# Performance work log

Hardware: AMD Instinct MI355X
Metric: run time of the kernel (lower is better)

The kernel has to match this reference:

```python
import jax, jax.numpy as jnp
import numpy as np
from jax import lax

N, C, A, H, W = 32, 512, 256, 64, 64

def _maxpool2(t):
    # 2x2 max pool, stride 2, NCHW
    return lax.reduce_window(t, -jnp.inf, lax.max, (1, 1, 2, 2), (1, 1, 2, 2), 'VALID')

def setup_inputs() -> dict:
    key = jax.random.key(0)
    ks = jax.random.split(key, 5)
    return {
        'x': jax.random.normal(ks[0], (N, C, H, W), dtype=jnp.float32),
        'w_g': jax.random.normal(ks[1], (A, C), dtype=jnp.float32) * 0.02,
        'b_g': jax.random.normal(ks[2], (A,), dtype=jnp.float32) * 0.02,
        'w_phi': jax.random.normal(ks[3], (A, C), dtype=jnp.float32) * 0.02,
        'b_phi': jax.random.normal(ks[4], (A,), dtype=jnp.float32) * 0.02,
    }

def reference(x, w_g, b_g, w_phi, b_phi):
    n, c, h, w = x.shape
    # g: 1x1 conv in->attn, flattened spatial: (N, A, H*W)
    g_x = (jnp.einsum('nchw,ac->nahw', x, w_g) + b_g[None, :, None, None]).reshape(n, A, h * w)
    # theta: maxpool of x, (N, C, HW/4)
    theta_x = _maxpool2(x).reshape(n, c, -1)
    # phi: 1x1 conv then maxpool, (N, HW/4, A)
    phi_conv = jnp.einsum('nchw,ac->nahw', x, w_phi) + b_phi[None, :, None, None]
    phi_x = _maxpool2(phi_conv).reshape(n, A, -1)  # (N, A, HW/4)
    # channel-attention scores: (N, C, A)
    cmat = jnp.einsum('ncm,nam->nca', theta_x, phi_x)
    attn = jax.nn.softmax(cmat, axis=-1)
    # aggregate: (N, C, HW)
    y = jnp.einsum('nca,nal->ncl', attn, g_x)
    z = y.reshape(n, c, h, w)
    return z + x
```

## Files before the change

### kernel.cpp

```cpp
#include <hip/hip_runtime.h>


typedef _Float16 half8 __attribute__((ext_vector_type(8)));
typedef _Float16 half4v __attribute__((ext_vector_type(4)));
typedef float f32x4 __attribute__((ext_vector_type(4)));

#define NB 32
#define CD 512
#define AD 256
#define PD 4096
#define PPD 1024

#define OFF_XT    0UL
#define OFF_WC    134217728UL
#define OFF_THETA 134742016UL
#define OFF_GT    168296448UL
#define OFF_PHI   235405312UL
#define OFF_ATTN  252182528UL

__global__ __launch_bounds__(256) void k_prep_w(const float* __restrict__ w_g,
                                                const float* __restrict__ w_phi,
                                                _Float16* __restrict__ Wc) {
    int idx4 = blockIdx.x * 256 + threadIdx.x;
    int flat = idx4 * 4;
    const float* src = (flat < AD * CD) ? (w_g + flat) : (w_phi + (flat - AD * CD));
    float4 v = *(const float4*)src;
    half4v h;
    h[0] = (_Float16)v.x; h[1] = (_Float16)v.y; h[2] = (_Float16)v.z; h[3] = (_Float16)v.w;
    *(half4v*)(Wc + flat) = h;
}

__global__ __launch_bounds__(256) void k_prep_x(const float* __restrict__ x,
                                                _Float16* __restrict__ xT,
                                                _Float16* __restrict__ theta) {
    __shared__ _Float16 tile[32 * 136];
    int pb = blockIdx.x;
    int cb = blockIdx.y;
    int n  = blockIdx.z;
    int t  = threadIdx.x;
    int p0 = pb * 128, c0 = cb * 32;

    const float* xbase = x + ((size_t)n * CD + c0) * PD + p0;
#pragma unroll
    for (int i = 0; i < 4; ++i) {
        int idx = i * 256 + t;
        int cl = idx >> 5;
        int ch = idx & 31;
        float4 v = *(const float4*)(xbase + (size_t)cl * PD + ch * 4);
        half4v h;
        h[0] = (_Float16)v.x; h[1] = (_Float16)v.y; h[2] = (_Float16)v.z; h[3] = (_Float16)v.w;
        *(half4v*)&tile[cl * 136 + ch * 4] = h;
    }
    __syncthreads();

    {
        int pl = t >> 1, ch = t & 1;
        _Float16 vals[16] __attribute__((aligned(16)));
#pragma unroll
        for (int j = 0; j < 16; ++j) vals[j] = tile[(ch * 16 + j) * 136 + pl];
        _Float16* dst = xT + ((size_t)n * PD + p0 + pl) * CD + c0 + ch * 16;
        *(uint4*)dst       = *(uint4*)&vals[0];
        *(uint4*)(dst + 8) = *(uint4*)&vals[8];
    }
    {
        int cl = t >> 3, u0 = (t & 7) * 4;
        _Float16 o[4] __attribute__((aligned(8)));
#pragma unroll
        for (int j = 0; j < 4; ++j) {
            int w2 = (u0 + j) * 2;
            float a0 = (float)tile[cl * 136 + w2];
            float a1 = (float)tile[cl * 136 + w2 + 1];
            float a2 = (float)tile[cl * 136 + 64 + w2];
            float a3 = (float)tile[cl * 136 + 64 + w2 + 1];
            o[j] = (_Float16)fmaxf(fmaxf(a0, a1), fmaxf(a2, a3));
        }
        _Float16* dst = theta + ((size_t)n * CD + c0 + cl) * PPD + pb * 32 + u0;
        *(uint2*)dst = *(uint2*)&o[0];
    }
}

__global__ __launch_bounds__(256) void k_gemm1(const _Float16* __restrict__ Wc,
                                               const _Float16* __restrict__ xT,
                                               const float* __restrict__ b_g,
                                               const float* __restrict__ b_phi,
                                               _Float16* __restrict__ gT,
                                               _Float16* __restrict__ phi) {
    __shared__ _Float16 smem[17408];
    _Float16* As = smem;
    _Float16* Bs = smem + 5120;

    int pb = blockIdx.x, ab = blockIdx.y, n = blockIdx.z;
    int a0 = ab * 128, p0 = pb * 128;
    int t = threadIdx.x;
    int w = t >> 6, l = t & 63;
    int ln = l & 15, q = l >> 4;
    int mw = (w >> 1) * 64, nw = (w & 1) * 64;

    const f32x4 vzero = {0.f, 0.f, 0.f, 0.f};
    f32x4 acc[4][4];
#pragma unroll
    for (int i = 0; i < 4; ++i)
#pragma unroll
        for (int j = 0; j < 4; ++j) acc[i][j] = vzero;

    const _Float16* Abase = Wc + (size_t)a0 * CD;
    const _Float16* Bbase = xT + ((size_t)n * PD + p0) * CD;

    for (int k0 = 0; k0 < 512; k0 += 32) {
#pragma unroll
        for (int i = 0; i < 2; ++i) {
            int idx = i * 256 + t;
            int row = idx >> 2, ch = idx & 3;
            *(half8*)&As[row * 40 + ch * 8] = *(const half8*)(Abase + (size_t)row * CD + k0 + ch * 8);
            *(half8*)&Bs[row * 40 + ch * 8] = *(const half8*)(Bbase + (size_t)row * CD + k0 + ch * 8);
        }
        __syncthreads();
        half8 af[4], bf[4];
#pragma unroll
        for (int mt = 0; mt < 4; ++mt) af[mt] = *(const half8*)&As[(mw + mt * 16 + ln) * 40 + q * 8];
#pragma unroll
        for (int nt = 0; nt < 4; ++nt) bf[nt] = *(const half8*)&Bs[(nw + nt * 16 + ln) * 40 + q * 8];
#pragma unroll
        for (int mt = 0; mt < 4; ++mt)
#pragma unroll
            for (int nt = 0; nt < 4; ++nt)
                acc[mt][nt] = __builtin_amdgcn_mfma_f32_16x16x32_f16(af[mt], bf[nt], acc[mt][nt], 0, 0, 0);
        __syncthreads();
    }

    bool is_g = (a0 < 256);
    const float* bias = is_g ? b_g : b_phi;
    int abase = a0 - (is_g ? 0 : 256);
    float bv[4][4];
#pragma unroll
    for (int mt = 0; mt < 4; ++mt)
#pragma unroll
        for (int r = 0; r < 4; ++r) bv[mt][r] = bias[abase + mw + mt * 16 + q * 4 + r];

    _Float16* T = smem;
    if (is_g) {
#pragma unroll
        for (int mt = 0; mt < 4; ++mt)
#pragma unroll
            for (int nt = 0; nt < 4; ++nt)
#pragma unroll
                for (int r = 0; r < 4; ++r) {
                    int al = mw + mt * 16 + q * 4 + r;
                    int pl = nw + nt * 16 + ln;
                    T[pl * 136 + al] = (_Float16)(acc[mt][nt][r] + bv[mt][r]);
                }
        __syncthreads();
#pragma unroll
        for (int i = 0; i < 8; ++i) {
            int idx = i * 256 + t;
            int pl = idx >> 4, ch = idx & 15;
            uint4 v = *(uint4*)&T[pl * 136 + ch * 8];
            *(uint4*)(gT + ((size_t)n * PD + p0 + pl) * AD + a0 + ch * 8) = v;
        }
    } else {
#pragma unroll
        for (int mt = 0; mt < 4; ++mt)
#pragma unroll
            for (int nt = 0; nt < 4; ++nt)
#pragma unroll
                for (int r = 0; r < 4; ++r) {
                    int al = mw + mt * 16 + q * 4 + r;
                    int pl = nw + nt * 16 + ln;
                    T[al * 136 + pl] = (_Float16)(acc[mt][nt][r] + bv[mt][r]);
                }
        __syncthreads();
        int al = t >> 1, hf = t & 1;
        _Float16 o[16] __attribute__((aligned(16)));
#pragma unroll
        for (int j = 0; j < 16; ++j) {
            int u = hf * 16 + j;
            float v0 = (float)T[al * 136 + 2 * u];
            float v1 = (float)T[al * 136 + 2 * u + 1];
            float v2 = (float)T[al * 136 + 64 + 2 * u];
            float v3 = (float)T[al * 136 + 64 + 2 * u + 1];
            o[j] = (_Float16)fmaxf(fmaxf(v0, v1), fmaxf(v2, v3));
        }
        _Float16* dst = phi + ((size_t)n * AD + (a0 - 256) + al) * PPD + pb * 32 + hf * 16;
        *(uint4*)dst       = *(uint4*)&o[0];
        *(uint4*)(dst + 8) = *(uint4*)&o[8];
    }
}

__global__ __launch_bounds__(256) void k_gemm2(const _Float16* __restrict__ theta,
                                               const _Float16* __restrict__ phi,
                                               _Float16* __restrict__ attn) {
    int cb = blockIdx.x;
    int n  = blockIdx.y;
    int t = threadIdx.x, w = t >> 6, l = t & 63;
    int ln = l & 15, q = l >> 4;
    int c0 = cb * 64 + w * 16;

    const _Float16* Ab = theta + ((size_t)n * CD + c0 + ln) * PPD;
    const _Float16* Bb = phi + ((size_t)n * AD + ln) * PPD;

    const f32x4 vzero = {0.f, 0.f, 0.f, 0.f};
    f32x4 acc[16];
#pragma unroll
    for (int i = 0; i < 16; ++i) acc[i] = vzero;

    for (int k0 = 0; k0 < 1024; k0 += 32) {
        half8 af = *(const half8*)(Ab + k0 + q * 8);
#pragma unroll
        for (int nt = 0; nt < 16; ++nt) {
            half8 bf = *(const half8*)(Bb + (size_t)nt * 16 * PPD + k0 + q * 8);
            acc[nt] = __builtin_amdgcn_mfma_f32_16x16x32_f16(af, bf, acc[nt], 0, 0, 0);
        }
    }

#pragma unroll
    for (int r = 0; r < 4; ++r) {
        float m = -1e30f;
#pragma unroll
        for (int nt = 0; nt < 16; ++nt) m = fmaxf(m, acc[nt][r]);
#pragma unroll
        for (int s = 1; s < 16; s <<= 1) m = fmaxf(m, __shfl_xor(m, s, 64));
        float sum = 0.f;
#pragma unroll
        for (int nt = 0; nt < 16; ++nt) {
            float e = __expf(acc[nt][r] - m);
            acc[nt][r] = e;
            sum += e;
        }
#pragma unroll
        for (int s = 1; s < 16; s <<= 1) sum += __shfl_xor(sum, s, 64);
        float inv = 1.0f / sum;
        int c = c0 + q * 4 + r;
        _Float16* dst = attn + ((size_t)n * CD + c) * AD + ln;
#pragma unroll
        for (int nt = 0; nt < 16; ++nt) dst[nt * 16] = (_Float16)(acc[nt][r] * inv);
    }
}

__global__ __launch_bounds__(256) void k_gemm3(const _Float16* __restrict__ attn,
                                               const _Float16* __restrict__ gT,
                                               const float* __restrict__ x,
                                               float* __restrict__ out) {
    __shared__ _Float16 smem[10240];
    _Float16* As = smem;
    _Float16* Bs = smem + 5120;

    int pb = blockIdx.x, cb = blockIdx.y, n = blockIdx.z;
    int c0 = cb * 128, p0 = pb * 128;
    int t = threadIdx.x;
    int w = t >> 6, l = t & 63;
    int ln = l & 15, q = l >> 4;
    int mw = (w >> 1) * 64, nw = (w & 1) * 64;

    const f32x4 vzero = {0.f, 0.f, 0.f, 0.f};
    f32x4 acc[4][4];
#pragma unroll
    for (int i = 0; i < 4; ++i)
#pragma unroll
        for (int j = 0; j < 4; ++j) acc[i][j] = vzero;

    const _Float16* Abase = attn + ((size_t)n * CD + c0) * AD;
    const _Float16* Bbase = gT + ((size_t)n * PD + p0) * AD;

    for (int k0 = 0; k0 < 256; k0 += 32) {
#pragma unroll
        for (int i = 0; i < 2; ++i) {
            int idx = i * 256 + t;
            int row = idx >> 2, ch = idx & 3;
            *(half8*)&As[row * 40 + ch * 8] = *(const half8*)(Abase + (size_t)row * AD + k0 + ch * 8);
            *(half8*)&Bs[row * 40 + ch * 8] = *(const half8*)(Bbase + (size_t)row * AD + k0 + ch * 8);
        }
        __syncthreads();
        half8 af[4], bf[4];
#pragma unroll
        for (int mt = 0; mt < 4; ++mt) af[mt] = *(const half8*)&Bs[(mw + mt * 16 + ln) * 40 + q * 8];
#pragma unroll
        for (int nt = 0; nt < 4; ++nt) bf[nt] = *(const half8*)&As[(nw + nt * 16 + ln) * 40 + q * 8];
#pragma unroll
        for (int mt = 0; mt < 4; ++mt)
#pragma unroll
            for (int nt = 0; nt < 4; ++nt)
                acc[mt][nt] = __builtin_amdgcn_mfma_f32_16x16x32_f16(af[mt], bf[nt], acc[mt][nt], 0, 0, 0);
        __syncthreads();
    }

#pragma unroll
    for (int mt = 0; mt < 4; ++mt) {
        int p = p0 + mw + mt * 16 + q * 4;
#pragma unroll
        for (int nt = 0; nt < 4; ++nt) {
            int c = c0 + nw + nt * 16 + ln;
            size_t off = ((size_t)n * CD + c) * PD + p;
            f32x4 xv = *(const f32x4*)(x + off);
            *(f32x4*)(out + off) = acc[mt][nt] + xv;
        }
    }
}

extern "C" void kernel_launch(void* const* d_in, const int* in_sizes, int n_in,
                              void* d_out, int out_size, void* d_ws, size_t ws_size,
                              hipStream_t stream) {
    const float* x     = (const float*)d_in[0];
    const float* w_g   = (const float*)d_in[1];
    const float* b_g   = (const float*)d_in[2];
    const float* w_phi = (const float*)d_in[3];
    const float* b_phi = (const float*)d_in[4];
    float* out = (float*)d_out;

    char* ws = (char*)d_ws;
    _Float16* xT    = (_Float16*)(ws + OFF_XT);
    _Float16* Wc    = (_Float16*)(ws + OFF_WC);
    _Float16* theta = (_Float16*)(ws + OFF_THETA);
    _Float16* gT    = (_Float16*)(ws + OFF_GT);
    _Float16* phi   = (_Float16*)(ws + OFF_PHI);
    _Float16* attn  = (_Float16*)(ws + OFF_ATTN);

    k_prep_w<<<dim3(256), 256, 0, stream>>>(w_g, w_phi, Wc);
    k_prep_x<<<dim3(32, 16, 32), 256, 0, stream>>>(x, xT, theta);
    k_gemm1<<<dim3(32, 4, 32), 256, 0, stream>>>(Wc, xT, b_g, b_phi, gT, phi);
    k_gemm2<<<dim3(8, 32), 256, 0, stream>>>(theta, phi, attn);
    k_gemm3<<<dim3(32, 4, 32), 256, 0, stream>>>(attn, gT, x, out);
}
```

Baseline: 827.5 us.

## Double-buffer GEMM tiles via direct global-to-LDS loads and split-K attention scores

The two large GEMM kernels now stage A/B tiles with global_load_lds into XOR-swizzled, double-buffered LDS, so the next K-slice is fetched while MFMAs consume the current one. This removes register round-trips and LDS bank conflicts. The score GEMM now splits K across the four waves with an LDS reduction before the softmax, which quadruples the number of blocks to fill the GPU. The cost is more LDS use and extra synchronization, and correctness depends on the load/wait ordering.

New measurement: 778.6 us. -5.9%, faster.

```diff
diff --git a/kernel.cpp b/kernel.cpp
--- a/kernel.cpp
+++ b/kernel.cpp
@@ -17,6 +17,30 @@
 #define OFF_GT    168296448UL
 #define OFF_PHI   235405312UL
 #define OFF_ATTN  252182528UL
+
+#define GLOAD16(gp, lp) \
+    __builtin_amdgcn_global_load_lds((const __attribute__((address_space(1))) void*)(gp), \
+                                     (__attribute__((address_space(3))) void*)(lp), 16, 0, 0)
+
+__device__ __forceinline__ int swz_off(int row, int q) {
+    return row * 32 + ((q ^ ((row >> 1) & 3)) * 8);
+}
+
+template <int LD>
+__device__ __forceinline__ void stage2(const _Float16* __restrict__ Ab,
+                                       const _Float16* __restrict__ Bb,
+                                       int k0, _Float16* bufA, _Float16* bufB, int t) {
+#pragma unroll
+    for (int j = 0; j < 4; ++j) {
+        int idx = j * 256 + t;
+        int ci = idx & 511;
+        int row = ci >> 2, chP = ci & 3;
+        int chL = chP ^ ((row >> 1) & 3);
+        const _Float16* src = ((idx < 512) ? Ab : Bb) + (size_t)row * LD + k0 + chL * 8;
+        _Float16* dst = ((idx < 512) ? bufA : bufB) + ci * 8;
+        GLOAD16(src, dst);
+    }
+}
 
 __global__ __launch_bounds__(256) void k_prep_w(const float* __restrict__ w_g,
                                                 const float* __restrict__ w_phi,
@@ -86,8 +110,6 @@
                                                _Float16* __restrict__ gT,
                                                _Float16* __restrict__ phi) {
     __shared__ _Float16 smem[17408];
-    _Float16* As = smem;
-    _Float16* Bs = smem + 5120;
 
     int pb = blockIdx.x, ab = blockIdx.y, n = blockIdx.z;
     int a0 = ab * 128, p0 = pb * 128;
@@ -106,20 +128,20 @@
     const _Float16* Abase = Wc + (size_t)a0 * CD;
     const _Float16* Bbase = xT + ((size_t)n * PD + p0) * CD;
 
-    for (int k0 = 0; k0 < 512; k0 += 32) {
-#pragma unroll
-        for (int i = 0; i < 2; ++i) {
-            int idx = i * 256 + t;
-            int row = idx >> 2, ch = idx & 3;
-            *(half8*)&As[row * 40 + ch * 8] = *(const half8*)(Abase + (size_t)row * CD + k0 + ch * 8);
-            *(half8*)&Bs[row * 40 + ch * 8] = *(const half8*)(Bbase + (size_t)row * CD + k0 + ch * 8);
-        }
-        __syncthreads();
+    stage2<CD>(Abase, Bbase, 0, smem, smem + 4096, t);
+    __syncthreads();
+
+    for (int ks = 0; ks < 16; ++ks) {
+        int oc = (ks & 1) << 13;
+        int on = oc ^ 8192;
+        if (ks < 15) stage2<CD>(Abase, Bbase, (ks + 1) * 32, smem + on, smem + on + 4096, t);
+        _Float16* As = smem + oc;
+        _Float16* Bs = smem + oc + 4096;
         half8 af[4], bf[4];
 #pragma unroll
-        for (int mt = 0; mt < 4; ++mt) af[mt] = *(const half8*)&As[(mw + mt * 16 + ln) * 40 + q * 8];
-#pragma unroll
-        for (int nt = 0; nt < 4; ++nt) bf[nt] = *(const half8*)&Bs[(nw + nt * 16 + ln) * 40 + q * 8];
+        for (int mt = 0; mt < 4; ++mt) af[mt] = *(const half8*)&As[swz_off(mw + mt * 16 + ln, q)];
+#pragma unroll
+        for (int nt = 0; nt < 4; ++nt) bf[nt] = *(const half8*)&Bs[swz_off(nw + nt * 16 + ln, q)];
 #pragma unroll
         for (int mt = 0; mt < 4; ++mt)
 #pragma unroll
@@ -189,21 +211,22 @@
 __global__ __launch_bounds__(256) void k_gemm2(const _Float16* __restrict__ theta,
                                                const _Float16* __restrict__ phi,
                                                _Float16* __restrict__ attn) {
+    __shared__ float red[3 * 64 * 65];
     int cb = blockIdx.x;
     int n  = blockIdx.y;
     int t = threadIdx.x, w = t >> 6, l = t & 63;
     int ln = l & 15, q = l >> 4;
-    int c0 = cb * 64 + w * 16;
-
-    const _Float16* Ab = theta + ((size_t)n * CD + c0 + ln) * PPD;
-    const _Float16* Bb = phi + ((size_t)n * AD + ln) * PPD;
+    int c0 = cb * 16;
+
+    const _Float16* Ab = theta + ((size_t)n * CD + c0 + ln) * PPD + w * 256;
+    const _Float16* Bb = phi + ((size_t)n * AD + ln) * PPD + w * 256;
 
     const f32x4 vzero = {0.f, 0.f, 0.f, 0.f};
     f32x4 acc[16];
 #pragma unroll
     for (int i = 0; i < 16; ++i) acc[i] = vzero;
 
-    for (int k0 = 0; k0 < 1024; k0 += 32) {
+    for (int k0 = 0; k0 < 256; k0 += 32) {
         half8 af = *(const half8*)(Ab + k0 + q * 8);
 #pragma unroll
         for (int nt = 0; nt < 16; ++nt) {
@@ -212,27 +235,45 @@
         }
     }
 
-#pragma unroll
-    for (int r = 0; r < 4; ++r) {
-        float m = -1e30f;
-#pragma unroll
-        for (int nt = 0; nt < 16; ++nt) m = fmaxf(m, acc[nt][r]);
-#pragma unroll
-        for (int s = 1; s < 16; s <<= 1) m = fmaxf(m, __shfl_xor(m, s, 64));
-        float sum = 0.f;
-#pragma unroll
-        for (int nt = 0; nt < 16; ++nt) {
-            float e = __expf(acc[nt][r] - m);
-            acc[nt][r] = e;
-            sum += e;
-        }
-#pragma unroll
-        for (int s = 1; s < 16; s <<= 1) sum += __shfl_xor(sum, s, 64);
-        float inv = 1.0f / sum;
-        int c = c0 + q * 4 + r;
-        _Float16* dst = attn + ((size_t)n * CD + c) * AD + ln;
-#pragma unroll
-        for (int nt = 0; nt < 16; ++nt) dst[nt * 16] = (_Float16)(acc[nt][r] * inv);
+    if (w > 0) {
+        float* dst = red + (w - 1) * 64 * 65 + l * 65;
+#pragma unroll
+        for (int nt = 0; nt < 16; ++nt)
+#pragma unroll
+            for (int r = 0; r < 4; ++r) dst[nt * 4 + r] = acc[nt][r];
+    }
+    __syncthreads();
+    if (w == 0) {
+#pragma unroll
+        for (int j = 0; j < 3; ++j) {
+            const float* src = red + j * 64 * 65 + l * 65;
+#pragma unroll
+            for (int nt = 0; nt < 16; ++nt)
+#pragma unroll
+                for (int r = 0; r < 4; ++r) acc[nt][r] += src[nt * 4 + r];
+        }
+#pragma unroll
+        for (int r = 0; r < 4; ++r) {
+            float m = -1e30f;
+#pragma unroll
+            for (int nt = 0; nt < 16; ++nt) m = fmaxf(m, acc[nt][r]);
+#pragma unroll
+            for (int s = 1; s < 16; s <<= 1) m = fmaxf(m, __shfl_xor(m, s, 64));
+            float sum = 0.f;
+#pragma unroll
+            for (int nt = 0; nt < 16; ++nt) {
+                float e = __expf(acc[nt][r] - m);
+                acc[nt][r] = e;
+                sum += e;
+            }
+#pragma unroll
+            for (int s = 1; s < 16; s <<= 1) sum += __shfl_xor(sum, s, 64);
+            float inv = 1.0f / sum;
+            int c = c0 + q * 4 + r;
+            _Float16* dst = attn + ((size_t)n * CD + c) * AD + ln;
+#pragma unroll
+            for (int nt = 0; nt < 16; ++nt) dst[nt * 16] = (_Float16)(acc[nt][r] * inv);
+        }
     }
 }
 
@@ -240,9 +281,7 @@
                                                const _Float16* __restrict__ gT,
                                                const float* __restrict__ x,
                                                float* __restrict__ out) {
-    __shared__ _Float16 smem[10240];
-    _Float16* As = smem;
-    _Float16* Bs = smem + 5120;
+    __shared__ _Float16 smem[16384];
 
     int pb = blockIdx.x, cb = blockIdx.y, n = blockIdx.z;
     int c0 = cb * 128, p0 = pb * 128;
@@ -261,20 +300,20 @@
     const _Float16* Abase = attn + ((size_t)n * CD + c0) * AD;
     const _Float16* Bbase = gT + ((size_t)n * PD + p0) * AD;
 
-    for (int k0 = 0; k0 < 256; k0 += 32) {
-#pragma unroll
-        for (int i = 0; i < 2; ++i) {
-            int idx = i * 256 + t;
-            int row = idx >> 2, ch = idx & 3;
-            *(half8*)&As[row * 40 + ch * 8] = *(const half8*)(Abase + (size_t)row * AD + k0 + ch * 8);
-            *(half8*)&Bs[row * 40 + ch * 8] = *(const half8*)(Bbase + (size_t)row * AD + k0 + ch * 8);
-        }
-        __syncthreads();
+    stage2<AD>(Abase, Bbase, 0, smem, smem + 4096, t);
+    __syncthreads();
+
+    for (int ks = 0; ks < 8; ++ks) {
+        int oc = (ks & 1) << 13;
+        int on = oc ^ 8192;
+        if (ks < 7) stage2<AD>(Abase, Bbase, (ks + 1) * 32, smem + on, smem + on + 4096, t);
+        _Float16* As = smem + oc;
+        _Float16* Bs = smem + oc + 4096;
         half8 af[4], bf[4];
 #pragma unroll
-        for (int mt = 0; mt < 4; ++mt) af[mt] = *(const half8*)&Bs[(mw + mt * 16 + ln) * 40 + q * 8];
-#pragma unroll
-        for (int nt = 0; nt < 4; ++nt) bf[nt] = *(const half8*)&As[(nw + nt * 16 + ln) * 40 + q * 8];
+        for (int mt = 0; mt < 4; ++mt) af[mt] = *(const half8*)&Bs[swz_off(mw + mt * 16 + ln, q)];
+#pragma unroll
+        for (int nt = 0; nt < 4; ++nt) bf[nt] = *(const half8*)&As[swz_off(nw + nt * 16 + ln, q)];
 #pragma unroll
         for (int mt = 0; mt < 4; ++mt)
 #pragma unroll
@@ -317,6 +356,6 @@
     k_prep_w<<<dim3(256), 256, 0, stream>>>(w_g, w_phi, Wc);
     k_prep_x<<<dim3(32, 16, 32), 256, 0, stream>>>(x, xT, theta);
     k_gemm1<<<dim3(32, 4, 32), 256, 0, stream>>>(Wc, xT, b_g, b_phi, gT, phi);
-    k_gemm2<<<dim3(8, 32), 256, 0, stream>>>(theta, phi, attn);
+    k_gemm2<<<dim3(32, 32), 256, 0, stream>>>(theta, phi, attn);
     k_gemm3<<<dim3(32, 4, 32), 256, 0, stream>>>(attn, gT, x, out);
 }
```
